# Kernel tuning notes

Hardware: AMD Instinct MI355X
Metric: run time of the kernel (lower is better)

## Reference

```python
import jax, jax.numpy as jnp
import numpy as np

B, TQ, TK = 32, 2000, 512
BLANK_LOGPROB = -1.0
NEG = -1e9  # stand-in for -inf, safe under logsumexp grads


def setup_inputs() -> dict:
    key = jax.random.key(0)
    k1, k2, k3 = jax.random.split(key, 3)
    attn_logprob = jax.random.normal(k1, (B, TQ, TK), dtype=jnp.float32)
    in_lens = jax.random.randint(k2, (B,), 1, TK + 1, dtype=jnp.int32)
    # query (mel) lengths >= key (text) lengths so the CTC alignment exists
    out_lens = jax.random.randint(k3, (B,), TK, TQ + 1, dtype=jnp.int32)
    return {"attn_logprob": attn_logprob, "in_lens": in_lens, "out_lens": out_lens}


def _forward_sum_loss(attn_logprob, in_lens, out_lens):
    # attn_logprob: [B, Tq, Tk]
    Bb, Tq, Tk = attn_logprob.shape
    kl = jnp.clip(in_lens, 1, Tk).astype(jnp.int32)      # target lengths
    ql = jnp.clip(out_lens, 1, Tq).astype(jnp.int32)     # input lengths

    # pad a blank column at key index 0 (blank logit = blank_logprob)
    padded = jnp.pad(attn_logprob, ((0, 0), (0, 0), (1, 0)),
                     constant_values=BLANK_LOGPROB)       # [B, Tq, Tk+1]
    # per-sample log_softmax over the first kl+1 key entries (masked softmax)
    key_mask = jnp.arange(Tk + 1)[None, :] <= kl[:, None]  # [B, Tk+1]
    logp = jax.nn.log_softmax(jnp.where(key_mask[:, None, :], padded, NEG), axis=-1)

    # CTC with targets = [1..kl] (all distinct), blank = 0.
    # Extended state sequence: blank,1,blank,2,...,blank,kl,blank -> 2*kl+1 states.
    S = 2 * Tk + 1
    s = jnp.arange(S)
    label_idx = jnp.where(s % 2 == 1, (s + 1) // 2, 0)          # emission index per state
    state_valid = s[None, :] < (2 * kl[:, None] + 1)            # [B, S]
    skip_ok = (s % 2 == 1) & (s >= 2)                           # distinct labels -> skip allowed

    e0 = logp[:, 0, label_idx]                                  # [B, S]
    alpha0 = jnp.full((Bb, S), NEG, dtype=logp.dtype)
    alpha0 = alpha0.at[:, 0].set(e0[:, 0]).at[:, 1].set(e0[:, 1])

    def step(alpha, xs):
        logp_t, t = xs                                          # logp_t: [B, Tk+1]
        e_t = logp_t[:, label_idx]                              # [B, S]
        p0 = alpha
        p1 = jnp.pad(alpha[:, :-1], ((0, 0), (1, 0)), constant_values=NEG)
        p2 = jnp.pad(alpha[:, :-2], ((0, 0), (2, 0)), constant_values=NEG)
        p2 = jnp.where(skip_ok[None, :], p2, NEG)
        new = jax.nn.logsumexp(jnp.stack([p0, p1, p2]), axis=0) + e_t
        new = jnp.where(state_valid, new, NEG)
        alpha = jnp.where((t < ql)[:, None], new, alpha)        # freeze past each ql
        return alpha, None

    xs = (jnp.moveaxis(logp[:, 1:, :], 0, 1), jnp.arange(1, Tq))
    alpha, _ = jax.lax.scan(step, alpha0, xs)

    end = 2 * kl                                                # final blank state
    a_end = jnp.take_along_axis(alpha, end[:, None], axis=1)[:, 0]
    a_lab = jnp.take_along_axis(alpha, (end - 1)[:, None], axis=1)[:, 0]
    ll = jnp.logaddexp(a_end, a_lab)
    # torch CTCLoss(reduction='mean') with batch 1 divides by target length
    loss = -ll / kl.astype(attn_logprob.dtype)
    return jnp.mean(loss)


def reference(attn_logprob, in_lens, out_lens):
    return _forward_sum_loss(attn_logprob, in_lens, out_lens)
```

## Files before the change

### kernel.cpp

```cpp
#include <hip/hip_runtime.h>
#include <math.h>

#define BB 32
#define TQQ 2000
#define TKK 512
#define CR 8
#define RS 8
#define NW 8
#define SLOT_F 520
#define BRN 32

__device__ __forceinline__ float dpp_mv_111(float x, float old) {
    return __int_as_float(__builtin_amdgcn_update_dpp(__float_as_int(old), __float_as_int(x), 0x111, 0xf, 0xf, false));
}
__device__ __forceinline__ float dpp_mv_112(float x, float old) {
    return __int_as_float(__builtin_amdgcn_update_dpp(__float_as_int(old), __float_as_int(x), 0x112, 0xf, 0xf, false));
}
__device__ __forceinline__ float dpp_mv_114(float x, float old) {
    return __int_as_float(__builtin_amdgcn_update_dpp(__float_as_int(old), __float_as_int(x), 0x114, 0xf, 0xf, false));
}
__device__ __forceinline__ float dpp_mv_118(float x, float old) {
    return __int_as_float(__builtin_amdgcn_update_dpp(__float_as_int(old), __float_as_int(x), 0x118, 0xf, 0xf, false));
}
__device__ __forceinline__ float dpp_mv_b15(float x, float old) {
    return __int_as_float(__builtin_amdgcn_update_dpp(__float_as_int(old), __float_as_int(x), 0x142, 0xf, 0xf, false));
}
__device__ __forceinline__ float dpp_mv_b31(float x, float old) {
    return __int_as_float(__builtin_amdgcn_update_dpp(__float_as_int(old), __float_as_int(x), 0x143, 0xf, 0xf, false));
}
__device__ __forceinline__ float dpp_wave_shr1(float x, float old) {
    return __int_as_float(__builtin_amdgcn_update_dpp(__float_as_int(old), __float_as_int(x), 0x138, 0xf, 0xf, false));
}

__device__ __forceinline__ float wred_max(float x) {
    x = fmaxf(x, dpp_mv_111(x, -1e38f));
    x = fmaxf(x, dpp_mv_112(x, -1e38f));
    x = fmaxf(x, dpp_mv_114(x, -1e38f));
    x = fmaxf(x, dpp_mv_118(x, -1e38f));
    x = fmaxf(x, dpp_mv_b15(x, -1e38f));
    x = fmaxf(x, dpp_mv_b31(x, -1e38f));
    return __int_as_float(__builtin_amdgcn_readlane(__float_as_int(x), 63));
}
__device__ __forceinline__ float wred_sum(float x) {
    x += dpp_mv_111(x, 0.0f);
    x += dpp_mv_112(x, 0.0f);
    x += dpp_mv_114(x, 0.0f);
    x += dpp_mv_118(x, 0.0f);
    x += dpp_mv_b15(x, 0.0f);
    x += dpp_mv_b31(x, 0.0f);
    return __int_as_float(__builtin_amdgcn_readlane(__float_as_int(x), 63));
}

__device__ __forceinline__ float pow2i(int e) {
    return __int_as_float((unsigned)(e + 127) << 23);
}

__device__ __forceinline__ void step_quad(float4 p, float pb, float o_prev,
                                          float E[4], float O[4]) {
    float t3 = E[3] + O[2];  O[3] = (O[3] + t3) * p.w;  E[3] = t3 * pb;
    float t2 = E[2] + O[1];  O[2] = (O[2] + t2) * p.z;  E[2] = t2 * pb;
    float t1 = E[1] + O[0];  O[1] = (O[1] + t1) * p.y;  E[1] = t1 * pb;
    float t0 = E[0] + o_prev; O[0] = (O[0] + t0) * p.x; E[0] = t0 * pb;
}

__global__ __launch_bounds__(NW * 64)
void ForwardSumLoss_77378130805413_kernel(const float* __restrict__ attn,
                                          const int* __restrict__ in_lens,
                                          const int* __restrict__ out_lens,
                                          float* __restrict__ out)
{
    __shared__ float s_slots[RS * CR * SLOT_F];
    __shared__ float s_dumpE[513];
    __shared__ float s_dumpO[512];
    __shared__ float s_bring[BRN];
    __shared__ int   s_ef0[4];
    __shared__ int   s_ready[RS];
    __shared__ int   s_w0, s_w1;
    __shared__ int   s_e0c, s_e1c;

    const int b    = blockIdx.x;
    const int tid  = threadIdx.x;
    const int wave = tid >> 6;
    const int lane = tid & 63;

    int kl = in_lens[b];  kl = kl < 1 ? 1 : (kl > TKK ? TKK : kl);
    int ql = out_lens[b]; ql = ql < 1 ? 1 : (ql > TQQ ? TQQ : ql);
    const int nchunks = (ql + CR - 1) / CR;

    if (tid < RS)  s_ready[tid] = -1;
    if (tid < BRN) s_bring[tid] = 0.f;
    if (tid == 32) s_w0 = -1;
    if (tid == 33) s_w1 = -1;
    __syncthreads();

    volatile int* vready = s_ready;
    volatile int* vw0    = &s_w0;
    volatile int* vw1    = &s_w1;
    volatile int* vEF0   = s_ef0;

    const float T = 1.0995116e12f;

    if (wave == 0) {
        __builtin_amdgcn_s_setprio(3);
        float E[4] = {0,0,0,0}, O[4] = {0,0,0,0};
        int e0c = 0;
        const int base4 = 4 * lane;
        int rdyN = -9, w1s = -9;

        for (int k = 0; k < nchunks; ++k) {
            const int t0   = k * CR;
            const int rows = min(ql - t0, CR);
            if (k >= 2) { while (w1s < k - 2) { w1s = *vw1; } }
            if (rdyN != k) { while (vready[k & (RS - 1)] != k) {} }
            asm volatile("" ::: "memory");
            const float* bp = s_slots + (size_t)(k & (RS - 1)) * CR * SLOT_F;

            if (rows == CR) {
                float4 P[CR]; float PB[CR];
                #pragma unroll
                for (int r = 0; r < CR; ++r) {
                    P[r]  = *(const float4*)(bp + r * SLOT_F + base4);
                    PB[r] = bp[r * SLOT_F + 512];
                }
                rdyN = vready[(k + 1) & (RS - 1)];
                w1s  = *vw1;
                #pragma unroll
                for (int r = 0; r < CR; ++r) {
                    if (k == 0 && r == 0) {
                        E[0] = (lane == 0) ? PB[0]  * T : 0.f;
                        O[0] = (lane == 0) ? P[0].x * T : 0.f;
                    } else {
                        float o_prev = dpp_wave_shr1(O[3], 0.0f);
                        step_quad(P[r], PB[r], o_prev, E, O);
                    }
                    if (r < CR - 1) { if (lane == 63) s_bring[(t0 + r) & (BRN - 1)] = O[3]; }
                }
                float m0 = fmaxf(fmaxf(fmaxf(E[0], E[1]), fmaxf(E[2], E[3])),
                                 fmaxf(fmaxf(O[0], O[1]), fmaxf(O[2], O[3])));
                m0 = wred_max(m0);
                int ef = 0;
                if (m0 > 0.f) ef = 167 - (int)((__float_as_uint(m0) >> 23) & 255);
                float fh = pow2i(ef - (ef >> 1));
                float fl = pow2i(ef >> 1);
                #pragma unroll
                for (int i = 0; i < 4; ++i) { E[i] = (E[i] * fh) * fl; O[i] = (O[i] * fh) * fl; }
                e0c += ef;
                if (lane == 0) vEF0[k & 3] = ef;
                if (lane == 63) s_bring[(t0 + CR - 1) & (BRN - 1)] = O[3];
            } else {
                for (int r = 0; r < rows; ++r) {
                    const float* sq = bp + r * SLOT_F;
                    float4 p = *(const float4*)(sq + base4);
                    float pb = sq[512];
                    if (k == 0 && r == 0) {
                        E[0] = (lane == 0) ? pb  * T : 0.f;
                        O[0] = (lane == 0) ? p.x * T : 0.f;
                    } else {
                        float o_prev = dpp_wave_shr1(O[3], 0.0f);
                        step_quad(p, pb, o_prev, E, O);
                    }
                    if (lane == 63) s_bring[(t0 + r) & (BRN - 1)] = O[3];
                }
            }
            asm volatile("" ::: "memory");
            if (lane == 0) *vw0 = k;
        }
        #pragma unroll
        for (int i = 0; i < 4; ++i) {
            s_dumpE[base4 + i] = E[i];
            s_dumpO[base4 + i] = O[i];
        }
        if (lane == 0) s_e0c = e0c;
    } else if (wave == 1) {
        __builtin_amdgcn_s_setprio(3);
        float E[4] = {0,0,0,0}, O[4] = {0,0,0,0}, e512 = 0.f;
        int e0c = 0, e1c = 0;
        const int base4 = 256 + 4 * lane;
        int w0s = -9;

        for (int k = 0; k < nchunks; ++k) {
            const int t0   = k * CR;
            const int rows = min(ql - t0, CR);
            while (w0s < k) { w0s = *vw0; }
            asm volatile("" ::: "memory");
            const float* bp = s_slots + (size_t)(k & (RS - 1)) * CR * SLOT_F;

            int dE = e1c - e0c;
            dE = dE < -250 ? -250 : (dE > 250 ? 250 : dE);
            const float Ch = pow2i(dE - (dE >> 1));
            const float Cl = pow2i(dE >> 1);

            if (rows == CR) {
                float4 P[CR]; float PB[CR], BND[CR];
                #pragma unroll
                for (int r = 0; r < CR; ++r) {
                    P[r]   = *(const float4*)(bp + r * SLOT_F + base4);
                    PB[r]  = bp[r * SLOT_F + 512];
                    BND[r] = (s_bring[(t0 - 1 + r) & (BRN - 1)] * Ch) * Cl;
                }
                w0s = *vw0;
                #pragma unroll
                for (int r = 0; r < CR; ++r) {
                    float o_prev = dpp_wave_shr1(O[3], 0.0f);
                    o_prev = (lane == 0) ? BND[r] : o_prev;
                    float te = e512 + O[3]; e512 = te * PB[r];
                    step_quad(P[r], PB[r], o_prev, E, O);
                }
                float m1 = fmaxf(fmaxf(fmaxf(E[0], E[1]), fmaxf(E[2], E[3])),
                                 fmaxf(fmaxf(O[0], O[1]), fmaxf(O[2], O[3])));
                m1 = fmaxf(m1, e512);
                m1 = wred_max(m1);
                int ef0k = vEF0[k & 3];
                int ef1  = (m1 > 0.f) ? (167 - (int)((__float_as_uint(m1) >> 23) & 255))
                                      : ef0k;
                float fh = pow2i(ef1 - (ef1 >> 1));
                float fl = pow2i(ef1 >> 1);
                #pragma unroll
                for (int i = 0; i < 4; ++i) { E[i] = (E[i] * fh) * fl; O[i] = (O[i] * fh) * fl; }
                e512 = (e512 * fh) * fl;
                e1c += ef1;
                e0c += ef0k;
            } else {
                for (int r = 0; r < rows; ++r) {
                    const float* sq = bp + r * SLOT_F;
                    float4 p = *(const float4*)(sq + base4);
                    float pb = sq[512];
                    float bnd = (s_bring[(t0 - 1 + r) & (BRN - 1)] * Ch) * Cl;
                    float o_prev = dpp_wave_shr1(O[3], 0.0f);
                    o_prev = (lane == 0) ? bnd : o_prev;
                    float te = e512 + O[3]; e512 = te * pb;
                    step_quad(p, pb, o_prev, E, O);
                }
            }
            asm volatile("" ::: "memory");
            if (lane == 0) *vw1 = k;
        }
        #pragma unroll
        for (int i = 0; i < 4; ++i) {
            s_dumpE[base4 + i] = E[i];
            s_dumpO[base4 + i] = O[i];
        }
        if (lane == 63) s_dumpE[512] = e512;
        if (lane == 0)  s_e1c = e1c;
    } else {
        const int pidx = wave - 2;
        const float* base = attn + (size_t)b * TQQ * TKK;
        const int j0 = 8 * lane;

        for (int c = pidx; c < nchunks; c += NW - 2) {
            const int t0 = c * CR;
            while (*vw1 < c - RS) { __builtin_amdgcn_s_sleep(4); }
            asm volatile("" ::: "memory");

            float4 x0[CR], x1[CR];
            #pragma unroll
            for (int r = 0; r < CR; ++r) {
                x0[r] = make_float4(-1e30f, -1e30f, -1e30f, -1e30f);
                x1[r] = x0[r];
                const int t = t0 + r;
                if (t < ql) {
                    const float* row = base + (size_t)t * TKK;
                    if (j0 < kl)     x0[r] = *(const float4*)(row + j0);
                    if (j0 + 4 < kl) x1[r] = *(const float4*)(row + j0 + 4);
                }
            }
            float* bp = s_slots + (size_t)(c & (RS - 1)) * CR * SLOT_F;
            #pragma unroll
            for (int r = 0; r < CR; ++r) {
                const int t = t0 + r;
                if (t >= ql) continue;
                float va[8] = {x0[r].x, x0[r].y, x0[r].z, x0[r].w,
                               x1[r].x, x1[r].y, x1[r].z, x1[r].w};
                float m = -1.0f;
                #pragma unroll
                for (int cc = 0; cc < 8; ++cc) if (j0 + cc < kl) m = fmaxf(m, va[cc]);
                m = wred_max(m);
                float pv[8]; float vsum = 0.f;
                #pragma unroll
                for (int cc = 0; cc < 8; ++cc) {
                    pv[cc] = (j0 + cc < kl) ? __expf(va[cc] - m) : 0.f;
                    vsum += pv[cc];
                }
                vsum = wred_sum(vsum);
                float vb   = __expf(-1.0f - m);
                float rinv = 1.0f / (vsum + vb);
                float* sp = bp + (size_t)r * SLOT_F;
                *(float4*)(sp + j0)     = make_float4(pv[0]*rinv, pv[1]*rinv, pv[2]*rinv, pv[3]*rinv);
                *(float4*)(sp + j0 + 4) = make_float4(pv[4]*rinv, pv[5]*rinv, pv[6]*rinv, pv[7]*rinv);
                if (lane == 0) sp[512] = vb * rinv;
            }
            __threadfence_block();
            if (lane == 0) vready[c & (RS - 1)] = c;
        }
    }

    __syncthreads();
    if (tid == 0) {
        const double logTd = 27.725887222397812;
        const double LN2d  = 0.69314718055994531;
        float aE = s_dumpE[kl];
        float aO = s_dumpO[kl - 1];
        int e0c = s_e0c, e1c = s_e1c;
        double sE = logTd + (double)((kl     >= 256) ? e1c : e0c) * LN2d;
        double sO = logTd + (double)((kl - 1 >= 256) ? e1c : e0c) * LN2d;
        double lE = (aE > 0.f) ? log((double)aE) - sE : -1e300;
        double lO = (aO > 0.f) ? log((double)aO) - sO : -1e300;
        double mx = fmax(lE, lO);
        double ll = (mx < -1e290) ? -745.0 : mx + log(exp(lE - mx) + exp(lO - mx));
        float val = (float)(-ll / ((double)kl * (double)BB));
        atomicAdd(out, val);
    }
}

extern "C" void kernel_launch(void* const* d_in, const int* in_sizes, int n_in,
                              void* d_out, int out_size, void* d_ws, size_t ws_size,
                              hipStream_t stream) {
    const float* attn     = (const float*)d_in[0];
    const int*   in_lens  = (const int*)d_in[1];
    const int*   out_lens = (const int*)d_in[2];
    float* out = (float*)d_out;
    hipMemsetAsync(out, 0, sizeof(float), stream);
    hipLaunchKernelGGL(ForwardSumLoss_77378130805413_kernel,
                       dim3(BB), dim3(NW * 64), 0, stream,
                       attn, in_lens, out_lens, out);
}
```

Baseline: 370.5 us.

## Split softmax into a parallel pre-pass kernel and slim the DP kernel

Adds a separate, fully parallel kernel that computes the masked softmax probabilities for every (batch, time) row and writes them to a workspace buffer. A second two-wave DP kernel then runs the CTC recurrence, prefetching four chunks of precomputed probabilities from the workspace. This takes the exp and reduction work off the serial per-batch critical path, which previously ran inside the single fused kernel alongside producer waves. In exchange the intermediate (about 130 MB) makes a round trip through global memory, and there is an extra launch. The original kernel stays as a fallback when no workspace is available.

Result: slower. 521.1 us (+40.6%).

```diff
diff --git a/kernel.cpp b/kernel.cpp
--- a/kernel.cpp
+++ b/kernel.cpp
@@ -9,6 +9,8 @@
 #define NW 8
 #define SLOT_F 520
 #define BRN 32
+#define WSROW 520
+#define SMC 4
 
 __device__ __forceinline__ float dpp_mv_111(float x, float old) {
     return __int_as_float(__builtin_amdgcn_update_dpp(__float_as_int(old), __float_as_int(x), 0x111, 0xf, 0xf, false));
@@ -61,6 +63,300 @@
     float t2 = E[2] + O[1];  O[2] = (O[2] + t2) * p.z;  E[2] = t2 * pb;
     float t1 = E[1] + O[0];  O[1] = (O[1] + t1) * p.y;  E[1] = t1 * pb;
     float t0 = E[0] + o_prev; O[0] = (O[0] + t0) * p.x; E[0] = t0 * pb;
+}
+
+__device__ __forceinline__ float4 selp4(float4 p, int m0, int kl) {
+    p.x = (m0 + 0 < kl) ? p.x : 0.f;
+    p.y = (m0 + 1 < kl) ? p.y : 0.f;
+    p.z = (m0 + 2 < kl) ? p.z : 0.f;
+    p.w = (m0 + 3 < kl) ? p.w : 0.f;
+    return p;
+}
+
+__global__ __launch_bounds__(64 * SMC)
+void ForwardSumLoss_77378130805413_softmax(const float* __restrict__ attn,
+                                           const int* __restrict__ in_lens,
+                                           const int* __restrict__ out_lens,
+                                           float* __restrict__ ws)
+{
+    const int b    = blockIdx.x;
+    const int wave = threadIdx.x >> 6;
+    const int lane = threadIdx.x & 63;
+
+    int kl = in_lens[b];  kl = kl < 1 ? 1 : (kl > TKK ? TKK : kl);
+    int ql = out_lens[b]; ql = ql < 1 ? 1 : (ql > TQQ ? TQQ : ql);
+
+    const int t0 = (blockIdx.y * SMC + wave) * CR;
+    if (t0 >= ql) return;
+
+    const float* base = attn + (size_t)b * TQQ * TKK;
+    const int j0 = 8 * lane;
+
+    float4 x0[CR], x1[CR];
+    #pragma unroll
+    for (int r = 0; r < CR; ++r) {
+        x0[r] = make_float4(-1e30f, -1e30f, -1e30f, -1e30f);
+        x1[r] = x0[r];
+        const int t = t0 + r;
+        if (t < ql) {
+            const float* row = base + (size_t)t * TKK;
+            if (j0 < kl)     x0[r] = *(const float4*)(row + j0);
+            if (j0 + 4 < kl) x1[r] = *(const float4*)(row + j0 + 4);
+        }
+    }
+    #pragma unroll
+    for (int r = 0; r < CR; ++r) {
+        const int t = t0 + r;
+        if (t >= ql) continue;
+        float va[8] = {x0[r].x, x0[r].y, x0[r].z, x0[r].w,
+                       x1[r].x, x1[r].y, x1[r].z, x1[r].w};
+        float m = -1.0f;
+        #pragma unroll
+        for (int cc = 0; cc < 8; ++cc) if (j0 + cc < kl) m = fmaxf(m, va[cc]);
+        m = wred_max(m);
+        float pv[8]; float vsum = 0.f;
+        #pragma unroll
+        for (int cc = 0; cc < 8; ++cc) {
+            pv[cc] = (j0 + cc < kl) ? __expf(va[cc] - m) : 0.f;
+            vsum += pv[cc];
+        }
+        vsum = wred_sum(vsum);
+        float vb   = __expf(-1.0f - m);
+        float rinv = 1.0f / (vsum + vb);
+        float* wrow = ws + ((size_t)b * TQQ + t) * WSROW;
+        if (j0 < kl) {
+            *(float4*)(wrow + j0)     = make_float4(pv[0]*rinv, pv[1]*rinv, pv[2]*rinv, pv[3]*rinv);
+            *(float4*)(wrow + j0 + 4) = make_float4(pv[4]*rinv, pv[5]*rinv, pv[6]*rinv, pv[7]*rinv);
+        }
+        if (lane == 0) wrow[512] = vb * rinv;
+    }
+}
+
+struct CK { float4 P[CR]; float PB[CR]; };
+
+__device__ __forceinline__ void pf_chunk(CK& c, const float* __restrict__ wsb,
+                                         int k, int nchunks, int ql,
+                                         int base4, int kl) {
+    if (k >= nchunks) return;
+    const int t0 = k * CR;
+    #pragma unroll
+    for (int r = 0; r < CR; ++r) {
+        int t  = t0 + r;
+        int tc = t < ql ? t : (ql - 1);
+        const float* rp = wsb + (size_t)tc * WSROW;
+        c.P[r]  = selp4(*(const float4*)(rp + base4), base4, kl);
+        c.PB[r] = rp[512];
+    }
+}
+
+__global__ __launch_bounds__(128, 1)
+void ForwardSumLoss_77378130805413_dp(const float* __restrict__ ws,
+                                      const int* __restrict__ in_lens,
+                                      const int* __restrict__ out_lens,
+                                      float* __restrict__ out)
+{
+    __shared__ float s_dumpE[513];
+    __shared__ float s_dumpO[512];
+    __shared__ float s_bring[BRN];
+    __shared__ int   s_ef0[4];
+    __shared__ int   s_w0, s_w1;
+    __shared__ int   s_e0c, s_e1c;
+
+    const int b    = blockIdx.x;
+    const int tid  = threadIdx.x;
+    const int wave = tid >> 6;
+    const int lane = tid & 63;
+
+    int kl = in_lens[b];  kl = kl < 1 ? 1 : (kl > TKK ? TKK : kl);
+    int ql = out_lens[b]; ql = ql < 1 ? 1 : (ql > TQQ ? TQQ : ql);
+    const int nchunks = (ql + CR - 1) / CR;
+
+    if (tid < BRN) s_bring[tid] = 0.f;
+    if (tid == 32) s_w0 = -1;
+    if (tid == 33) s_w1 = -1;
+    __syncthreads();
+
+    volatile int* vw0  = &s_w0;
+    volatile int* vw1  = &s_w1;
+    volatile int* vEF0 = s_ef0;
+
+    const float T = 1.0995116e12f;
+    const float* wsb = ws + (size_t)b * TQQ * WSROW;
+
+    if (wave == 0) {
+        float E[4] = {0,0,0,0}, O[4] = {0,0,0,0};
+        int e0c = 0;
+        const int base4 = 4 * lane;
+        int w1s = -9;
+        int k = 0;
+
+        CK c0, c1, c2, c3;
+        pf_chunk(c0, wsb, 0, nchunks, ql, base4, kl);
+        pf_chunk(c1, wsb, 1, nchunks, ql, base4, kl);
+        pf_chunk(c2, wsb, 2, nchunks, ql, base4, kl);
+        pf_chunk(c3, wsb, 3, nchunks, ql, base4, kl);
+
+        auto body = [&](CK& c) {
+            const int t0   = k * CR;
+            const int rows = min(ql - t0, CR);
+            if (k >= 2) { while (w1s < k - 2) { w1s = *vw1; } }
+            asm volatile("" ::: "memory");
+            if (rows == CR) {
+                #pragma unroll
+                for (int r = 0; r < CR; ++r) {
+                    if (k == 0 && r == 0) {
+                        E[0] = (lane == 0) ? c.PB[0]  * T : 0.f;
+                        O[0] = (lane == 0) ? c.P[0].x * T : 0.f;
+                    } else {
+                        float o_prev = dpp_wave_shr1(O[3], 0.0f);
+                        step_quad(c.P[r], c.PB[r], o_prev, E, O);
+                    }
+                    if (r < CR - 1) { if (lane == 63) s_bring[(t0 + r) & (BRN - 1)] = O[3]; }
+                }
+                float m0 = fmaxf(fmaxf(fmaxf(E[0], E[1]), fmaxf(E[2], E[3])),
+                                 fmaxf(fmaxf(O[0], O[1]), fmaxf(O[2], O[3])));
+                m0 = wred_max(m0);
+                int ef = 0;
+                if (m0 > 0.f) ef = 167 - (int)((__float_as_uint(m0) >> 23) & 255);
+                float fh = pow2i(ef - (ef >> 1));
+                float fl = pow2i(ef >> 1);
+                #pragma unroll
+                for (int i = 0; i < 4; ++i) { E[i] = (E[i] * fh) * fl; O[i] = (O[i] * fh) * fl; }
+                e0c += ef;
+                if (lane == 0) vEF0[k & 3] = ef;
+                if (lane == 63) s_bring[(t0 + CR - 1) & (BRN - 1)] = O[3];
+            } else {
+                #pragma unroll
+                for (int r = 0; r < CR; ++r) {
+                    if (r < rows) {
+                        if (k == 0 && r == 0) {
+                            E[0] = (lane == 0) ? c.PB[0]  * T : 0.f;
+                            O[0] = (lane == 0) ? c.P[0].x * T : 0.f;
+                        } else {
+                            float o_prev = dpp_wave_shr1(O[3], 0.0f);
+                            step_quad(c.P[r], c.PB[r], o_prev, E, O);
+                        }
+                        if (lane == 63) s_bring[(t0 + r) & (BRN - 1)] = O[3];
+                    }
+                }
+            }
+            asm volatile("" ::: "memory");
+            if (lane == 0) *vw0 = k;
+            pf_chunk(c, wsb, k + 4, nchunks, ql, base4, kl);
+            w1s = *vw1;
+        };
+
+        while (k < nchunks) {
+            body(c0); if (++k >= nchunks) break;
+            body(c1); if (++k >= nchunks) break;
+            body(c2); if (++k >= nchunks) break;
+            body(c3); ++k;
+        }
+        #pragma unroll
+        for (int i = 0; i < 4; ++i) {
+            s_dumpE[base4 + i] = E[i];
+            s_dumpO[base4 + i] = O[i];
+        }
+        if (lane == 0) s_e0c = e0c;
+    } else if (wave == 1) {
+        float E[4] = {0,0,0,0}, O[4] = {0,0,0,0}, e512 = 0.f;
+        int e0c = 0, e1c = 0;
+        const int base4 = 256 + 4 * lane;
+        int w0s = -9;
+        int k = 0;
+
+        CK c0, c1, c2, c3;
+        pf_chunk(c0, wsb, 0, nchunks, ql, base4, kl);
+        pf_chunk(c1, wsb, 1, nchunks, ql, base4, kl);
+        pf_chunk(c2, wsb, 2, nchunks, ql, base4, kl);
+        pf_chunk(c3, wsb, 3, nchunks, ql, base4, kl);
+
+        auto body = [&](CK& c) {
+            const int t0   = k * CR;
+            const int rows = min(ql - t0, CR);
+            while (w0s < k) { w0s = *vw0; }
+            asm volatile("" ::: "memory");
+
+            int dE = e1c - e0c;
+            dE = dE < -250 ? -250 : (dE > 250 ? 250 : dE);
+            const float Ch = pow2i(dE - (dE >> 1));
+            const float Cl = pow2i(dE >> 1);
+
+            if (rows == CR) {
+                float BND[CR];
+                #pragma unroll
+                for (int r = 0; r < CR; ++r)
+                    BND[r] = (s_bring[(t0 - 1 + r) & (BRN - 1)] * Ch) * Cl;
+                #pragma unroll
+                for (int r = 0; r < CR; ++r) {
+                    float o_prev = dpp_wave_shr1(O[3], 0.0f);
+                    o_prev = (lane == 0) ? BND[r] : o_prev;
+                    float te = e512 + O[3]; e512 = te * c.PB[r];
+                    step_quad(c.P[r], c.PB[r], o_prev, E, O);
+                }
+                float m1 = fmaxf(fmaxf(fmaxf(E[0], E[1]), fmaxf(E[2], E[3])),
+                                 fmaxf(fmaxf(O[0], O[1]), fmaxf(O[2], O[3])));
+                m1 = fmaxf(m1, e512);
+                m1 = wred_max(m1);
+                int ef0k = vEF0[k & 3];
+                int ef1  = (m1 > 0.f) ? (167 - (int)((__float_as_uint(m1) >> 23) & 255))
+                                      : ef0k;
+                float fh = pow2i(ef1 - (ef1 >> 1));
+                float fl = pow2i(ef1 >> 1);
+                #pragma unroll
+                for (int i = 0; i < 4; ++i) { E[i] = (E[i] * fh) * fl; O[i] = (O[i] * fh) * fl; }
+                e512 = (e512 * fh) * fl;
+                e1c += ef1;
+                e0c += ef0k;
+            } else {
+                #pragma unroll
+                for (int r = 0; r < CR; ++r) {
+                    if (r < rows) {
+                        float bnd = (s_bring[(t0 - 1 + r) & (BRN - 1)] * Ch) * Cl;
+                        float o_prev = dpp_wave_shr1(O[3], 0.0f);
+                        o_prev = (lane == 0) ? bnd : o_prev;
+                        float te = e512 + O[3]; e512 = te * c.PB[r];
+                        step_quad(c.P[r], c.PB[r], o_prev, E, O);
+                    }
+                }
+            }
+            asm volatile("" ::: "memory");
+            if (lane == 0) *vw1 = k;
+            pf_chunk(c, wsb, k + 4, nchunks, ql, base4, kl);
+            w0s = *vw0;
+        };
+
+        while (k < nchunks) {
+            body(c0); if (++k >= nchunks) break;
+            body(c1); if (++k >= nchunks) break;
+            body(c2); if (++k >= nchunks) break;
+            body(c3); ++k;
+        }
+        #pragma unroll
+        for (int i = 0; i < 4; ++i) {
+            s_dumpE[base4 + i] = E[i];
+            s_dumpO[base4 + i] = O[i];
+        }
+        if (lane == 63) s_dumpE[512] = e512;
+        if (lane == 0)  s_e1c = e1c;
+    }
+
+    __syncthreads();
+    if (tid == 0) {
+        const double logTd = 27.725887222397812;
+        const double LN2d  = 0.69314718055994531;
+        float aE = s_dumpE[kl];
+        float aO = s_dumpO[kl - 1];
+        int e0c = s_e0c, e1c = s_e1c;
+        double sE = logTd + (double)((kl     >= 256) ? e1c : e0c) * LN2d;
+        double sO = logTd + (double)((kl - 1 >= 256) ? e1c : e0c) * LN2d;
+        double lE = (aE > 0.f) ? log((double)aE) - sE : -1e300;
+        double lO = (aO > 0.f) ? log((double)aO) - sO : -1e300;
+        double mx = fmax(lE, lO);
+        double ll = (mx < -1e290) ? -745.0 : mx + log(exp(lE - mx) + exp(lO - mx));
+        float val = (float)(-ll / ((double)kl * (double)BB));
+        atomicAdd(out, val);
+    }
 }
 
 __global__ __launch_bounds__(NW * 64)
@@ -320,7 +616,20 @@
     const int*   out_lens = (const int*)d_in[2];
     float* out = (float*)d_out;
     hipMemsetAsync(out, 0, sizeof(float), stream);
-    hipLaunchKernelGGL(ForwardSumLoss_77378130805413_kernel,
-                       dim3(BB), dim3(NW * 64), 0, stream,
-                       attn, in_lens, out_lens, out);
-}
+
+    const size_t need = (size_t)BB * TQQ * WSROW * sizeof(float);
+    if (d_ws != nullptr && ws_size >= need) {
+        float* ws = (float*)d_ws;
+        dim3 g1(BB, (TQQ + SMC * CR - 1) / (SMC * CR));
+        hipLaunchKernelGGL(ForwardSumLoss_77378130805413_softmax,
+                           g1, dim3(64 * SMC), 0, stream,
+                           attn, in_lens, out_lens, ws);
+        hipLaunchKernelGGL(ForwardSumLoss_77378130805413_dp,
+                           dim3(BB), dim3(128), 0, stream,
+                           (const float*)ws, in_lens, out_lens, out);
+    } else {
+        hipLaunchKernelGGL(ForwardSumLoss_77378130805413_kernel,
+                           dim3(BB), dim3(NW * 64), 0, stream,
+                           attn, in_lens, out_lens, out);
+    }
+}
```

## Merge two-wave CTC recurrence into one wave, freeing a wave for loading

Applied to the files above, without the earlier changes.

The alpha recurrence was split across two waves, one per half of the state vector, linked by a shared-memory boundary ring and separate exponent-scale counters. It now runs in a single wave that holds both halves in registers and passes the boundary value with readlane, which removes the cross-wave handshakes, the boundary ring and the scale reconciliation. The freed wave joins the producer pool, so seven waves now load and softmax rows. The trade-off is that each serial step does twice the arithmetic on one wave, which lengthens the critical path unless the removed synchronisation latency was the larger cost.

Result: slower. 417.7 us (+12.7%).

```diff
diff --git a/kernel.cpp b/kernel.cpp
--- a/kernel.cpp
+++ b/kernel.cpp
@@ -8,7 +8,6 @@
 #define RS 8
 #define NW 8
 #define SLOT_F 520
-#define BRN 32
 
 __device__ __forceinline__ float dpp_mv_111(float x, float old) {
     return __int_as_float(__builtin_amdgcn_update_dpp(__float_as_int(old), __float_as_int(x), 0x111, 0xf, 0xf, false));
@@ -72,11 +71,9 @@
     __shared__ float s_slots[RS * CR * SLOT_F];
     __shared__ float s_dumpE[513];
     __shared__ float s_dumpO[512];
-    __shared__ float s_bring[BRN];
-    __shared__ int   s_ef0[4];
     __shared__ int   s_ready[RS];
-    __shared__ int   s_w0, s_w1;
-    __shared__ int   s_e0c, s_e1c;
+    __shared__ int   s_w0;
+    __shared__ int   s_ec;
 
     const int b    = blockIdx.x;
     const int tid  = threadIdx.x;
@@ -88,168 +85,116 @@
     const int nchunks = (ql + CR - 1) / CR;
 
     if (tid < RS)  s_ready[tid] = -1;
-    if (tid < BRN) s_bring[tid] = 0.f;
     if (tid == 32) s_w0 = -1;
-    if (tid == 33) s_w1 = -1;
     __syncthreads();
 
     volatile int* vready = s_ready;
     volatile int* vw0    = &s_w0;
-    volatile int* vw1    = &s_w1;
-    volatile int* vEF0   = s_ef0;
 
     const float T = 1.0995116e12f;
 
     if (wave == 0) {
         __builtin_amdgcn_s_setprio(3);
-        float E[4] = {0,0,0,0}, O[4] = {0,0,0,0};
-        int e0c = 0;
-        const int base4 = 4 * lane;
-        int rdyN = -9, w1s = -9;
+        float El[4] = {0,0,0,0}, Ol[4] = {0,0,0,0};
+        float Eh[4] = {0,0,0,0}, Oh[4] = {0,0,0,0};
+        float e512 = 0.f;
+        int ec = 0;
+        const int b4 = 4 * lane;
+        int rdyN = -9;
 
         for (int k = 0; k < nchunks; ++k) {
             const int t0   = k * CR;
             const int rows = min(ql - t0, CR);
-            if (k >= 2) { while (w1s < k - 2) { w1s = *vw1; } }
             if (rdyN != k) { while (vready[k & (RS - 1)] != k) {} }
             asm volatile("" ::: "memory");
             const float* bp = s_slots + (size_t)(k & (RS - 1)) * CR * SLOT_F;
 
             if (rows == CR) {
-                float4 P[CR]; float PB[CR];
+                float4 PL[CR], PH[CR]; float PB[CR];
                 #pragma unroll
                 for (int r = 0; r < CR; ++r) {
-                    P[r]  = *(const float4*)(bp + r * SLOT_F + base4);
+                    PL[r] = *(const float4*)(bp + r * SLOT_F + b4);
+                    PH[r] = *(const float4*)(bp + r * SLOT_F + 256 + b4);
                     PB[r] = bp[r * SLOT_F + 512];
                 }
+                asm volatile("s_waitcnt lgkmcnt(0)" ::: "memory");
+                if (lane == 0) *vw0 = k;
                 rdyN = vready[(k + 1) & (RS - 1)];
-                w1s  = *vw1;
                 #pragma unroll
                 for (int r = 0; r < CR; ++r) {
                     if (k == 0 && r == 0) {
-                        E[0] = (lane == 0) ? PB[0]  * T : 0.f;
-                        O[0] = (lane == 0) ? P[0].x * T : 0.f;
+                        El[0] = (lane == 0) ? PB[0]  * T : 0.f;
+                        Ol[0] = (lane == 0) ? PL[0].x * T : 0.f;
                     } else {
-                        float o_prev = dpp_wave_shr1(O[3], 0.0f);
-                        step_quad(P[r], PB[r], o_prev, E, O);
+                        float olo3 = Ol[3], ohi3 = Oh[3];
+                        float o_lo = dpp_wave_shr1(olo3, 0.0f);
+                        float o_hi = dpp_wave_shr1(ohi3, 0.0f);
+                        float bl = __int_as_float(__builtin_amdgcn_readlane(__float_as_int(olo3), 63));
+                        o_hi = (lane == 0) ? bl : o_hi;
+                        float te = e512 + ohi3; e512 = te * PB[r];
+                        step_quad(PH[r], PB[r], o_hi, Eh, Oh);
+                        step_quad(PL[r], PB[r], o_lo, El, Ol);
                     }
-                    if (r < CR - 1) { if (lane == 63) s_bring[(t0 + r) & (BRN - 1)] = O[3]; }
-                }
-                float m0 = fmaxf(fmaxf(fmaxf(E[0], E[1]), fmaxf(E[2], E[3])),
-                                 fmaxf(fmaxf(O[0], O[1]), fmaxf(O[2], O[3])));
+                }
+                float m0 = fmaxf(fmaxf(fmaxf(El[0], El[1]), fmaxf(El[2], El[3])),
+                                 fmaxf(fmaxf(Ol[0], Ol[1]), fmaxf(Ol[2], Ol[3])));
+                float m1 = fmaxf(fmaxf(fmaxf(Eh[0], Eh[1]), fmaxf(Eh[2], Eh[3])),
+                                 fmaxf(fmaxf(Oh[0], Oh[1]), fmaxf(Oh[2], Oh[3])));
+                m0 = fmaxf(m0, m1);
+                m0 = fmaxf(m0, (lane == 63) ? e512 : 0.f);
                 m0 = wred_max(m0);
                 int ef = 0;
                 if (m0 > 0.f) ef = 167 - (int)((__float_as_uint(m0) >> 23) & 255);
                 float fh = pow2i(ef - (ef >> 1));
                 float fl = pow2i(ef >> 1);
                 #pragma unroll
-                for (int i = 0; i < 4; ++i) { E[i] = (E[i] * fh) * fl; O[i] = (O[i] * fh) * fl; }
-                e0c += ef;
-                if (lane == 0) vEF0[k & 3] = ef;
-                if (lane == 63) s_bring[(t0 + CR - 1) & (BRN - 1)] = O[3];
+                for (int i = 0; i < 4; ++i) {
+                    El[i] = (El[i] * fh) * fl; Ol[i] = (Ol[i] * fh) * fl;
+                    Eh[i] = (Eh[i] * fh) * fl; Oh[i] = (Oh[i] * fh) * fl;
+                }
+                e512 = (e512 * fh) * fl;
+                ec += ef;
             } else {
                 for (int r = 0; r < rows; ++r) {
                     const float* sq = bp + r * SLOT_F;
-                    float4 p = *(const float4*)(sq + base4);
+                    float4 pl = *(const float4*)(sq + b4);
+                    float4 ph = *(const float4*)(sq + 256 + b4);
                     float pb = sq[512];
                     if (k == 0 && r == 0) {
-                        E[0] = (lane == 0) ? pb  * T : 0.f;
-                        O[0] = (lane == 0) ? p.x * T : 0.f;
+                        El[0] = (lane == 0) ? pb   * T : 0.f;
+                        Ol[0] = (lane == 0) ? pl.x * T : 0.f;
                     } else {
-                        float o_prev = dpp_wave_shr1(O[3], 0.0f);
-                        step_quad(p, pb, o_prev, E, O);
+                        float olo3 = Ol[3], ohi3 = Oh[3];
+                        float o_lo = dpp_wave_shr1(olo3, 0.0f);
+                        float o_hi = dpp_wave_shr1(ohi3, 0.0f);
+                        float bl = __int_as_float(__builtin_amdgcn_readlane(__float_as_int(olo3), 63));
+                        o_hi = (lane == 0) ? bl : o_hi;
+                        float te = e512 + ohi3; e512 = te * pb;
+                        step_quad(ph, pb, o_hi, Eh, Oh);
+                        step_quad(pl, pb, o_lo, El, Ol);
                     }
-                    if (lane == 63) s_bring[(t0 + r) & (BRN - 1)] = O[3];
-                }
+                }
+                asm volatile("" ::: "memory");
+                if (lane == 0) *vw0 = k;
             }
-            asm volatile("" ::: "memory");
-            if (lane == 0) *vw0 = k;
         }
         #pragma unroll
         for (int i = 0; i < 4; ++i) {
-            s_dumpE[base4 + i] = E[i];
-            s_dumpO[base4 + i] = O[i];
-        }
-        if (lane == 0) s_e0c = e0c;
-    } else if (wave == 1) {
-        __builtin_amdgcn_s_setprio(3);
-        float E[4] = {0,0,0,0}, O[4] = {0,0,0,0}, e512 = 0.f;
-        int e0c = 0, e1c = 0;
-        const int base4 = 256 + 4 * lane;
-        int w0s = -9;
-
-        for (int k = 0; k < nchunks; ++k) {
-            const int t0   = k * CR;
-            const int rows = min(ql - t0, CR);
-            while (w0s < k) { w0s = *vw0; }
-            asm volatile("" ::: "memory");
-            const float* bp = s_slots + (size_t)(k & (RS - 1)) * CR * SLOT_F;
-
-            int dE = e1c - e0c;
-            dE = dE < -250 ? -250 : (dE > 250 ? 250 : dE);
-            const float Ch = pow2i(dE - (dE >> 1));
-            const float Cl = pow2i(dE >> 1);
-
-            if (rows == CR) {
-                float4 P[CR]; float PB[CR], BND[CR];
-                #pragma unroll
-                for (int r = 0; r < CR; ++r) {
-                    P[r]   = *(const float4*)(bp + r * SLOT_F + base4);
-                    PB[r]  = bp[r * SLOT_F + 512];
-                    BND[r] = (s_bring[(t0 - 1 + r) & (BRN - 1)] * Ch) * Cl;
-                }
-                w0s = *vw0;
-                #pragma unroll
-                for (int r = 0; r < CR; ++r) {
-                    float o_prev = dpp_wave_shr1(O[3], 0.0f);
-                    o_prev = (lane == 0) ? BND[r] : o_prev;
-                    float te = e512 + O[3]; e512 = te * PB[r];
-                    step_quad(P[r], PB[r], o_prev, E, O);
-                }
-                float m1 = fmaxf(fmaxf(fmaxf(E[0], E[1]), fmaxf(E[2], E[3])),
-                                 fmaxf(fmaxf(O[0], O[1]), fmaxf(O[2], O[3])));
-                m1 = fmaxf(m1, e512);
-                m1 = wred_max(m1);
-                int ef0k = vEF0[k & 3];
-                int ef1  = (m1 > 0.f) ? (167 - (int)((__float_as_uint(m1) >> 23) & 255))
-                                      : ef0k;
-                float fh = pow2i(ef1 - (ef1 >> 1));
-                float fl = pow2i(ef1 >> 1);
-                #pragma unroll
-                for (int i = 0; i < 4; ++i) { E[i] = (E[i] * fh) * fl; O[i] = (O[i] * fh) * fl; }
-                e512 = (e512 * fh) * fl;
-                e1c += ef1;
-                e0c += ef0k;
-            } else {
-                for (int r = 0; r < rows; ++r) {
-                    const float* sq = bp + r * SLOT_F;
-                    float4 p = *(const float4*)(sq + base4);
-                    float pb = sq[512];
-                    float bnd = (s_bring[(t0 - 1 + r) & (BRN - 1)] * Ch) * Cl;
-                    float o_prev = dpp_wave_shr1(O[3], 0.0f);
-                    o_prev = (lane == 0) ? bnd : o_prev;
-                    float te = e512 + O[3]; e512 = te * pb;
-                    step_quad(p, pb, o_prev, E, O);
-                }
-            }
-            asm volatile("" ::: "memory");
-            if (lane == 0) *vw1 = k;
-        }
-        #pragma unroll
-        for (int i = 0; i < 4; ++i) {
-            s_dumpE[base4 + i] = E[i];
-            s_dumpO[base4 + i] = O[i];
+            s_dumpE[b4 + i]       = El[i];
+            s_dumpO[b4 + i]       = Ol[i];
+            s_dumpE[256 + b4 + i] = Eh[i];
+            s_dumpO[256 + b4 + i] = Oh[i];
         }
         if (lane == 63) s_dumpE[512] = e512;
-        if (lane == 0)  s_e1c = e1c;
+        if (lane == 0)  s_ec = ec;
     } else {
-        const int pidx = wave - 2;
+        const int pidx = wave - 1;
         const float* base = attn + (size_t)b * TQQ * TKK;
         const int j0 = 8 * lane;
 
-        for (int c = pidx; c < nchunks; c += NW - 2) {
+        for (int c = pidx; c < nchunks; c += NW - 1) {
             const int t0 = c * CR;
-            while (*vw1 < c - RS) { __builtin_amdgcn_s_sleep(4); }
+            while (*vw0 < c - RS) { __builtin_amdgcn_s_sleep(4); }
             asm volatile("" ::: "memory");
 
             float4 x0[CR], x1[CR];
@@ -300,11 +245,10 @@
         const double LN2d  = 0.69314718055994531;
         float aE = s_dumpE[kl];
         float aO = s_dumpO[kl - 1];
-        int e0c = s_e0c, e1c = s_e1c;
-        double sE = logTd + (double)((kl     >= 256) ? e1c : e0c) * LN2d;
-        double sO = logTd + (double)((kl - 1 >= 256) ? e1c : e0c) * LN2d;
-        double lE = (aE > 0.f) ? log((double)aE) - sE : -1e300;
-        double lO = (aO > 0.f) ? log((double)aO) - sO : -1e300;
+        int ec = s_ec;
+        double sC = logTd + (double)ec * LN2d;
+        double lE = (aE > 0.f) ? log((double)aE) - sC : -1e300;
+        double lO = (aO > 0.f) ? log((double)aO) - sC : -1e300;
         double mx = fmax(lE, lO);
         double ll = (mx < -1e290) ? -745.0 : mx + log(exp(lE - mx) + exp(lO - mx));
         float val = (float)(-ll / ((double)kl * (double)BB));
```

## Double chunk size to 16 rows, halve ring slots, pack blank probs contiguously

Applied to the files above, without the earlier changes.

Each handoff chunk grows from 8 to 16 rows, with the ring shrunk from 8 to 4 slots, so the two recurrence waves spin on shared flags half as often. Per-row blank probabilities move into a separate contiguous array that is loaded with float4 reads instead of strided scalar reads. Rescaling still happens every 8 rows through an inner two-half loop, and the wave-0/wave-1 lag allowance widens to 3 chunks. The cost is coarser producer granularity, which can delay pipeline startup and leave less ring slack for the producer waves.

Measured after the change: 499.4 us. 1.35x slower.

```diff
diff --git a/kernel.cpp b/kernel.cpp
--- a/kernel.cpp
+++ b/kernel.cpp
@@ -4,11 +4,12 @@
 #define BB 32
 #define TQQ 2000
 #define TKK 512
-#define CR 8
-#define RS 8
+#define CR 16
+#define HR 8
+#define RS 4
 #define NW 8
 #define SLOT_F 520
-#define BRN 32
+#define BRN 64
 
 __device__ __forceinline__ float dpp_mv_111(float x, float old) {
     return __int_as_float(__builtin_amdgcn_update_dpp(__float_as_int(old), __float_as_int(x), 0x111, 0xf, 0xf, false));
@@ -70,10 +71,11 @@
                                           float* __restrict__ out)
 {
     __shared__ float s_slots[RS * CR * SLOT_F];
+    __shared__ float s_pbblk[RS * CR];
     __shared__ float s_dumpE[513];
     __shared__ float s_dumpO[512];
     __shared__ float s_bring[BRN];
-    __shared__ int   s_ef0[4];
+    __shared__ int   s_ef0[8];
     __shared__ int   s_ready[RS];
     __shared__ int   s_w0, s_w1;
     __shared__ int   s_e0c, s_e1c;
@@ -89,8 +91,8 @@
 
     if (tid < RS)  s_ready[tid] = -1;
     if (tid < BRN) s_bring[tid] = 0.f;
-    if (tid == 32) s_w0 = -1;
-    if (tid == 33) s_w1 = -1;
+    if (tid == 64) s_w0 = -1;
+    if (tid == 65) s_w1 = -1;
     __syncthreads();
 
     volatile int* vready = s_ready;
@@ -107,63 +109,71 @@
         const int base4 = 4 * lane;
         int rdyN = -9, w1s = -9;
 
-        for (int k = 0; k < nchunks; ++k) {
-            const int t0   = k * CR;
+        for (int kk = 0; kk < nchunks; ++kk) {
+            const int t0   = kk * CR;
             const int rows = min(ql - t0, CR);
-            if (k >= 2) { while (w1s < k - 2) { w1s = *vw1; } }
-            if (rdyN != k) { while (vready[k & (RS - 1)] != k) {} }
-            asm volatile("" ::: "memory");
-            const float* bp = s_slots + (size_t)(k & (RS - 1)) * CR * SLOT_F;
+            if (kk >= 3) { while (w1s < kk - 3) { w1s = *vw1; } }
+            if (rdyN != kk) { while (vready[kk & (RS - 1)] != kk) {} }
+            asm volatile("" ::: "memory");
+            const float* bp  = s_slots + (size_t)(kk & (RS - 1)) * CR * SLOT_F;
+            const float* pbb = s_pbblk + (kk & (RS - 1)) * CR;
 
             if (rows == CR) {
-                float4 P[CR]; float PB[CR];
-                #pragma unroll
-                for (int r = 0; r < CR; ++r) {
-                    P[r]  = *(const float4*)(bp + r * SLOT_F + base4);
-                    PB[r] = bp[r * SLOT_F + 512];
-                }
-                rdyN = vready[(k + 1) & (RS - 1)];
+                float4 PL[CR]; float PB[CR];
+                #pragma unroll
+                for (int r = 0; r < CR; ++r)
+                    PL[r] = *(const float4*)(bp + r * SLOT_F + base4);
+                #pragma unroll
+                for (int i = 0; i < CR / 4; ++i) {
+                    float4 v = *(const float4*)(pbb + 4 * i);
+                    PB[4*i+0] = v.x; PB[4*i+1] = v.y; PB[4*i+2] = v.z; PB[4*i+3] = v.w;
+                }
+                rdyN = vready[(kk + 1) & (RS - 1)];
                 w1s  = *vw1;
                 #pragma unroll
-                for (int r = 0; r < CR; ++r) {
-                    if (k == 0 && r == 0) {
-                        E[0] = (lane == 0) ? PB[0]  * T : 0.f;
-                        O[0] = (lane == 0) ? P[0].x * T : 0.f;
-                    } else {
-                        float o_prev = dpp_wave_shr1(O[3], 0.0f);
-                        step_quad(P[r], PB[r], o_prev, E, O);
-                    }
-                    if (r < CR - 1) { if (lane == 63) s_bring[(t0 + r) & (BRN - 1)] = O[3]; }
-                }
-                float m0 = fmaxf(fmaxf(fmaxf(E[0], E[1]), fmaxf(E[2], E[3])),
-                                 fmaxf(fmaxf(O[0], O[1]), fmaxf(O[2], O[3])));
-                m0 = wred_max(m0);
-                int ef = 0;
-                if (m0 > 0.f) ef = 167 - (int)((__float_as_uint(m0) >> 23) & 255);
-                float fh = pow2i(ef - (ef >> 1));
-                float fl = pow2i(ef >> 1);
-                #pragma unroll
-                for (int i = 0; i < 4; ++i) { E[i] = (E[i] * fh) * fl; O[i] = (O[i] * fh) * fl; }
-                e0c += ef;
-                if (lane == 0) vEF0[k & 3] = ef;
-                if (lane == 63) s_bring[(t0 + CR - 1) & (BRN - 1)] = O[3];
+                for (int h = 0; h < 2; ++h) {
+                    #pragma unroll
+                    for (int r = 0; r < HR; ++r) {
+                        const int rr = h * HR + r;
+                        if (kk == 0 && h == 0 && r == 0) {
+                            E[0] = (lane == 0) ? PB[0]   * T : 0.f;
+                            O[0] = (lane == 0) ? PL[0].x * T : 0.f;
+                        } else {
+                            float o_prev = dpp_wave_shr1(O[3], 0.0f);
+                            step_quad(PL[rr], PB[rr], o_prev, E, O);
+                        }
+                        if (r < HR - 1) { if (lane == 63) s_bring[(t0 + rr) & (BRN - 1)] = O[3]; }
+                    }
+                    float m0 = fmaxf(fmaxf(fmaxf(E[0], E[1]), fmaxf(E[2], E[3])),
+                                     fmaxf(fmaxf(O[0], O[1]), fmaxf(O[2], O[3])));
+                    m0 = wred_max(m0);
+                    int ef = 0;
+                    if (m0 > 0.f) ef = 167 - (int)((__float_as_uint(m0) >> 23) & 255);
+                    float fh = pow2i(ef - (ef >> 1));
+                    float fl = pow2i(ef >> 1);
+                    #pragma unroll
+                    for (int i = 0; i < 4; ++i) { E[i] = (E[i] * fh) * fl; O[i] = (O[i] * fh) * fl; }
+                    e0c += ef;
+                    if (lane == 0) vEF0[(2 * kk + h) & 7] = ef;
+                    if (lane == 63) s_bring[(t0 + h * HR + HR - 1) & (BRN - 1)] = O[3];
+                }
             } else {
                 for (int r = 0; r < rows; ++r) {
                     const float* sq = bp + r * SLOT_F;
-                    float4 p = *(const float4*)(sq + base4);
-                    float pb = sq[512];
-                    if (k == 0 && r == 0) {
-                        E[0] = (lane == 0) ? pb  * T : 0.f;
-                        O[0] = (lane == 0) ? p.x * T : 0.f;
+                    float4 pl = *(const float4*)(sq + base4);
+                    float pb = pbb[r];
+                    if (kk == 0 && r == 0) {
+                        E[0] = (lane == 0) ? pb   * T : 0.f;
+                        O[0] = (lane == 0) ? pl.x * T : 0.f;
                     } else {
                         float o_prev = dpp_wave_shr1(O[3], 0.0f);
-                        step_quad(p, pb, o_prev, E, O);
+                        step_quad(pl, pb, o_prev, E, O);
                     }
                     if (lane == 63) s_bring[(t0 + r) & (BRN - 1)] = O[3];
                 }
             }
             asm volatile("" ::: "memory");
-            if (lane == 0) *vw0 = k;
+            if (lane == 0) *vw0 = kk;
         }
         #pragma unroll
         for (int i = 0; i < 4; ++i) {
@@ -178,62 +188,76 @@
         const int base4 = 256 + 4 * lane;
         int w0s = -9;
 
-        for (int k = 0; k < nchunks; ++k) {
-            const int t0   = k * CR;
+        for (int kk = 0; kk < nchunks; ++kk) {
+            const int t0   = kk * CR;
             const int rows = min(ql - t0, CR);
-            while (w0s < k) { w0s = *vw0; }
-            asm volatile("" ::: "memory");
-            const float* bp = s_slots + (size_t)(k & (RS - 1)) * CR * SLOT_F;
-
-            int dE = e1c - e0c;
-            dE = dE < -250 ? -250 : (dE > 250 ? 250 : dE);
-            const float Ch = pow2i(dE - (dE >> 1));
-            const float Cl = pow2i(dE >> 1);
+            while (w0s < kk) { w0s = *vw0; }
+            asm volatile("" ::: "memory");
+            const float* bp  = s_slots + (size_t)(kk & (RS - 1)) * CR * SLOT_F;
+            const float* pbb = s_pbblk + (kk & (RS - 1)) * CR;
 
             if (rows == CR) {
-                float4 P[CR]; float PB[CR], BND[CR];
-                #pragma unroll
-                for (int r = 0; r < CR; ++r) {
-                    P[r]   = *(const float4*)(bp + r * SLOT_F + base4);
-                    PB[r]  = bp[r * SLOT_F + 512];
-                    BND[r] = (s_bring[(t0 - 1 + r) & (BRN - 1)] * Ch) * Cl;
+                float4 PL[CR]; float PB[CR];
+                #pragma unroll
+                for (int r = 0; r < CR; ++r)
+                    PL[r] = *(const float4*)(bp + r * SLOT_F + base4);
+                #pragma unroll
+                for (int i = 0; i < CR / 4; ++i) {
+                    float4 v = *(const float4*)(pbb + 4 * i);
+                    PB[4*i+0] = v.x; PB[4*i+1] = v.y; PB[4*i+2] = v.z; PB[4*i+3] = v.w;
                 }
                 w0s = *vw0;
                 #pragma unroll
-                for (int r = 0; r < CR; ++r) {
-                    float o_prev = dpp_wave_shr1(O[3], 0.0f);
-                    o_prev = (lane == 0) ? BND[r] : o_prev;
-                    float te = e512 + O[3]; e512 = te * PB[r];
-                    step_quad(P[r], PB[r], o_prev, E, O);
-                }
-                float m1 = fmaxf(fmaxf(fmaxf(E[0], E[1]), fmaxf(E[2], E[3])),
-                                 fmaxf(fmaxf(O[0], O[1]), fmaxf(O[2], O[3])));
-                m1 = fmaxf(m1, e512);
-                m1 = wred_max(m1);
-                int ef0k = vEF0[k & 3];
-                int ef1  = (m1 > 0.f) ? (167 - (int)((__float_as_uint(m1) >> 23) & 255))
-                                      : ef0k;
-                float fh = pow2i(ef1 - (ef1 >> 1));
-                float fl = pow2i(ef1 >> 1);
-                #pragma unroll
-                for (int i = 0; i < 4; ++i) { E[i] = (E[i] * fh) * fl; O[i] = (O[i] * fh) * fl; }
-                e512 = (e512 * fh) * fl;
-                e1c += ef1;
-                e0c += ef0k;
+                for (int h = 0; h < 2; ++h) {
+                    int dE = e1c - e0c;
+                    dE = dE < -250 ? -250 : (dE > 250 ? 250 : dE);
+                    const float Ch = pow2i(dE - (dE >> 1));
+                    const float Cl = pow2i(dE >> 1);
+                    int ef0k = vEF0[(2 * kk + h) & 7];
+                    float BND[HR];
+                    #pragma unroll
+                    for (int r = 0; r < HR; ++r)
+                        BND[r] = (s_bring[(t0 + h * HR - 1 + r) & (BRN - 1)] * Ch) * Cl;
+                    #pragma unroll
+                    for (int r = 0; r < HR; ++r) {
+                        const int rr = h * HR + r;
+                        float o_prev = dpp_wave_shr1(O[3], 0.0f);
+                        o_prev = (lane == 0) ? BND[r] : o_prev;
+                        float te = e512 + O[3]; e512 = te * PB[rr];
+                        step_quad(PL[rr], PB[rr], o_prev, E, O);
+                    }
+                    float m1 = fmaxf(fmaxf(fmaxf(E[0], E[1]), fmaxf(E[2], E[3])),
+                                     fmaxf(fmaxf(O[0], O[1]), fmaxf(O[2], O[3])));
+                    m1 = fmaxf(m1, e512);
+                    m1 = wred_max(m1);
+                    int ef1 = (m1 > 0.f) ? (167 - (int)((__float_as_uint(m1) >> 23) & 255))
+                                         : ef0k;
+                    float fh = pow2i(ef1 - (ef1 >> 1));
+                    float fl = pow2i(ef1 >> 1);
+                    #pragma unroll
+                    for (int i = 0; i < 4; ++i) { E[i] = (E[i] * fh) * fl; O[i] = (O[i] * fh) * fl; }
+                    e512 = (e512 * fh) * fl;
+                    e1c += ef1;
+                    e0c += ef0k;
+                }
             } else {
+                int dE = e1c - e0c;
+                dE = dE < -250 ? -250 : (dE > 250 ? 250 : dE);
+                const float Ch = pow2i(dE - (dE >> 1));
+                const float Cl = pow2i(dE >> 1);
                 for (int r = 0; r < rows; ++r) {
                     const float* sq = bp + r * SLOT_F;
-                    float4 p = *(const float4*)(sq + base4);
-                    float pb = sq[512];
+                    float4 pl = *(const float4*)(sq + base4);
+                    float pb = pbb[r];
                     float bnd = (s_bring[(t0 - 1 + r) & (BRN - 1)] * Ch) * Cl;
                     float o_prev = dpp_wave_shr1(O[3], 0.0f);
                     o_prev = (lane == 0) ? bnd : o_prev;
                     float te = e512 + O[3]; e512 = te * pb;
-                    step_quad(p, pb, o_prev, E, O);
+                    step_quad(pl, pb, o_prev, E, O);
                 }
             }
             asm volatile("" ::: "memory");
-            if (lane == 0) *vw1 = k;
+            if (lane == 0) *vw1 = kk;
         }
         #pragma unroll
         for (int i = 0; i < 4; ++i) {
@@ -248,46 +272,50 @@
         const int j0 = 8 * lane;
 
         for (int c = pidx; c < nchunks; c += NW - 2) {
-            const int t0 = c * CR;
+            const int tc0 = c * CR;
             while (*vw1 < c - RS) { __builtin_amdgcn_s_sleep(4); }
             asm volatile("" ::: "memory");
-
-            float4 x0[CR], x1[CR];
+            float* bp  = s_slots + (size_t)(c & (RS - 1)) * CR * SLOT_F;
+            float* pbb = s_pbblk + (c & (RS - 1)) * CR;
+
             #pragma unroll
-            for (int r = 0; r < CR; ++r) {
-                x0[r] = make_float4(-1e30f, -1e30f, -1e30f, -1e30f);
-                x1[r] = x0[r];
-                const int t = t0 + r;
-                if (t < ql) {
-                    const float* row = base + (size_t)t * TKK;
-                    if (j0 < kl)     x0[r] = *(const float4*)(row + j0);
-                    if (j0 + 4 < kl) x1[r] = *(const float4*)(row + j0 + 4);
-                }
-            }
-            float* bp = s_slots + (size_t)(c & (RS - 1)) * CR * SLOT_F;
-            #pragma unroll
-            for (int r = 0; r < CR; ++r) {
-                const int t = t0 + r;
-                if (t >= ql) continue;
-                float va[8] = {x0[r].x, x0[r].y, x0[r].z, x0[r].w,
-                               x1[r].x, x1[r].y, x1[r].z, x1[r].w};
-                float m = -1.0f;
-                #pragma unroll
-                for (int cc = 0; cc < 8; ++cc) if (j0 + cc < kl) m = fmaxf(m, va[cc]);
-                m = wred_max(m);
-                float pv[8]; float vsum = 0.f;
-                #pragma unroll
-                for (int cc = 0; cc < 8; ++cc) {
-                    pv[cc] = (j0 + cc < kl) ? __expf(va[cc] - m) : 0.f;
-                    vsum += pv[cc];
-                }
-                vsum = wred_sum(vsum);
-                float vb   = __expf(-1.0f - m);
-                float rinv = 1.0f / (vsum + vb);
-                float* sp = bp + (size_t)r * SLOT_F;
-                *(float4*)(sp + j0)     = make_float4(pv[0]*rinv, pv[1]*rinv, pv[2]*rinv, pv[3]*rinv);
-                *(float4*)(sp + j0 + 4) = make_float4(pv[4]*rinv, pv[5]*rinv, pv[6]*rinv, pv[7]*rinv);
-                if (lane == 0) sp[512] = vb * rinv;
+            for (int h = 0; h < 2; ++h) {
+                float4 x0[HR], x1[HR];
+                #pragma unroll
+                for (int r = 0; r < HR; ++r) {
+                    x0[r] = make_float4(-1e30f, -1e30f, -1e30f, -1e30f);
+                    x1[r] = x0[r];
+                    const int t = tc0 + h * HR + r;
+                    if (t < ql) {
+                        const float* row = base + (size_t)t * TKK;
+                        if (j0 < kl)     x0[r] = *(const float4*)(row + j0);
+                        if (j0 + 4 < kl) x1[r] = *(const float4*)(row + j0 + 4);
+                    }
+                }
+                #pragma unroll
+                for (int r = 0; r < HR; ++r) {
+                    const int t = tc0 + h * HR + r;
+                    if (t >= ql) continue;
+                    float va[8] = {x0[r].x, x0[r].y, x0[r].z, x0[r].w,
+                                   x1[r].x, x1[r].y, x1[r].z, x1[r].w};
+                    float m = -1.0f;
+                    #pragma unroll
+                    for (int cc = 0; cc < 8; ++cc) if (j0 + cc < kl) m = fmaxf(m, va[cc]);
+                    m = wred_max(m);
+                    float pv[8]; float vsum = 0.f;
+                    #pragma unroll
+                    for (int cc = 0; cc < 8; ++cc) {
+                        pv[cc] = (j0 + cc < kl) ? __expf(va[cc] - m) : 0.f;
+                        vsum += pv[cc];
+                    }
+                    vsum = wred_sum(vsum);
+                    float vb   = __expf(-1.0f - m);
+                    float rinv = 1.0f / (vsum + vb);
+                    float* sp = bp + (size_t)(h * HR + r) * SLOT_F;
+                    *(float4*)(sp + j0)     = make_float4(pv[0]*rinv, pv[1]*rinv, pv[2]*rinv, pv[3]*rinv);
+                    *(float4*)(sp + j0 + 4) = make_float4(pv[4]*rinv, pv[5]*rinv, pv[6]*rinv, pv[7]*rinv);
+                    if (lane == 0) pbb[h * HR + r] = vb * rinv;
+                }
             }
             __threadfence_block();
             if (lane == 0) vready[c & (RS - 1)] = c;
```
